# Optimization experiments

Hardware: AMD Instinct MI355X
Metric: run time of the kernel (lower is better)

## Reference

```python
import jax, jax.numpy as jnp
import numpy as np

B, T, E, H = 8, 2048, 1024, 64

def setup_inputs() -> dict:
    key = jax.random.key(0)
    ks = jax.random.split(key, 7)
    s = 1.0 / np.sqrt(E)
    return {
        "x": jax.random.normal(ks[0], (B, T, E), dtype=jnp.float32),
        "Wk": jax.random.normal(ks[1], (E, H), dtype=jnp.float32) * s,
        "bk": jax.random.normal(ks[2], (H,), dtype=jnp.float32) * 0.01,
        "Wq": jax.random.normal(ks[3], (E, H), dtype=jnp.float32) * s,
        "bq": jax.random.normal(ks[4], (H,), dtype=jnp.float32) * 0.01,
        "Wv": jax.random.normal(ks[5], (E, H), dtype=jnp.float32) * s,
        "bv": jax.random.normal(ks[6], (H,), dtype=jnp.float32) * 0.01,
    }

def reference(x, Wk, bk, Wq, bq, Wv, bv):
    # q,k,v: [B, T, H]
    k = x @ Wk + bk
    q = x @ Wq + bq
    v = x @ Wv + bv
    scale = jnp.asarray(H, x.dtype) ** -0.5
    scores = jnp.einsum('bth,bsh->bts', q, k) * scale  # [B, T, T]
    T_ = x.shape[1]
    causal = jnp.tril(jnp.ones((T_, T_), dtype=bool))
    scores = jnp.where(causal, scores, jnp.asarray(-jnp.inf, x.dtype))
    attn = jax.nn.softmax(scores, axis=-1)  # dropout p=0.0 -> identity
    return jnp.einsum('bts,bsh->bth', attn, v)
```

## Files before the change

kernel.cpp:

```cpp
#include <hip/hip_runtime.h>
#include <hip/hip_bf16.h>
#include <math.h>

#define BB 8
#define TT 2048
#define EE 1024
#define HH 64
#define QSCALE 0.18033688011112042f

typedef __attribute__((ext_vector_type(8))) short short8;
typedef __attribute__((ext_vector_type(4))) float f32x4;
typedef __attribute__((ext_vector_type(4))) unsigned short us4;

__device__ inline unsigned short f2bf(float f) {
  union { __hip_bfloat16 h; unsigned short u; } cv;
  cv.h = __float2bfloat16(f);
  return cv.u;
}

__global__ __launch_bounds__(256) void prep_w(
    const float* __restrict__ Wk, const float* __restrict__ Wq,
    const float* __restrict__ Wv, unsigned short* __restrict__ Wf) {
  const int idx = blockIdx.x * 256 + threadIdx.x;
  const int lane = idx & 63, ks = (idx >> 6) & 31, t = idx >> 11;
  const int q = lane & 15, g = lane >> 4;
  const int m = t >> 2, h = (t & 3) * 16 + q;
  const float* W = (m == 0) ? Wk : (m == 1) ? Wq : Wv;
  const float sc = (m == 1) ? QSCALE : 1.f;
  const int e0 = ks * 32 + g * 8;
  unsigned short v[8];
  #pragma unroll
  for (int j = 0; j < 8; ++j) v[j] = f2bf(W[(e0 + j) * 64 + h] * sc);
  *(short8*)&Wf[(size_t)idx * 8] = *(short8*)v;
}

__global__ __launch_bounds__(256) void qkv_proj(
    const float* __restrict__ x,
    const float* __restrict__ bk, const float* __restrict__ bq,
    const float* __restrict__ bv, const unsigned short* __restrict__ Wf,
    unsigned short* __restrict__ kf, unsigned short* __restrict__ qf,
    unsigned short* __restrict__ vf) {
  __shared__ alignas(16) unsigned short xs[2][32][264];

  const int tid = threadIdx.x;
  const long row0 = (long)blockIdx.x * 32;
  const int w = tid >> 6, lane = tid & 63;
  const int q = lane & 15, g = lane >> 4;

  const float4* xg = (const float4*)&x[row0 * EE];

  #pragma unroll
  for (int i = 0; i < 8; ++i) {
    const int flat = i * 256 + tid;
    const int rr = flat >> 6, c4 = flat & 63;
    const float4 xv = xg[rr * 256 + c4];
    us4 pk = {f2bf(xv.x), f2bf(xv.y), f2bf(xv.z), f2bf(xv.w)};
    *(us4*)&xs[0][rr][c4 * 4] = pk;
  }
  __syncthreads();

  const f32x4 z = {0.f, 0.f, 0.f, 0.f};
  f32x4 acc00 = z, acc01 = z, acc02 = z;
  f32x4 acc10 = z, acc11 = z, acc12 = z;
  const unsigned short* wf0 = &Wf[(size_t)(3 * w) * 16384 + (size_t)lane * 8];

  float4 st[8];
  #pragma unroll
  for (int cc = 0; cc < 4; ++cc) {
    if (cc < 3) {
      #pragma unroll
      for (int i = 0; i < 8; ++i) {
        const int flat = i * 256 + tid;
        const int rr = flat >> 6, c4 = flat & 63;
        st[i] = xg[rr * 256 + (cc + 1) * 64 + c4];
      }
    }
    #pragma unroll
    for (int ksl = 0; ksl < 8; ++ksl) {
      const short8 a0 = *(const short8*)&xs[cc & 1][q][ksl * 32 + g * 8];
      const short8 a1 = *(const short8*)&xs[cc & 1][16 + q][ksl * 32 + g * 8];
      const int ks = cc * 8 + ksl;
      const short8 b0 = *(const short8*)&wf0[ks * 512];
      const short8 b1 = *(const short8*)&wf0[16384 + ks * 512];
      const short8 b2 = *(const short8*)&wf0[32768 + ks * 512];
      acc00 = __builtin_amdgcn_mfma_f32_16x16x32_bf16(a0, b0, acc00, 0, 0, 0);
      acc10 = __builtin_amdgcn_mfma_f32_16x16x32_bf16(a1, b0, acc10, 0, 0, 0);
      acc01 = __builtin_amdgcn_mfma_f32_16x16x32_bf16(a0, b1, acc01, 0, 0, 0);
      acc11 = __builtin_amdgcn_mfma_f32_16x16x32_bf16(a1, b1, acc11, 0, 0, 0);
      acc02 = __builtin_amdgcn_mfma_f32_16x16x32_bf16(a0, b2, acc02, 0, 0, 0);
      acc12 = __builtin_amdgcn_mfma_f32_16x16x32_bf16(a1, b2, acc12, 0, 0, 0);
    }
    if (cc < 3) {
      #pragma unroll
      for (int i = 0; i < 8; ++i) {
        const int flat = i * 256 + tid;
        const int rr = flat >> 6, c4 = flat & 63;
        us4 pk = {f2bf(st[i].x), f2bf(st[i].y), f2bf(st[i].z), f2bf(st[i].w)};
        *(us4*)&xs[(cc + 1) & 1][rr][c4 * 4] = pk;
      }
    }
    __syncthreads();
  }

  const long bidx = row0 >> 11;
  const int tl0 = (int)(row0 & 2047);
  #pragma unroll
  for (int i = 0; i < 3; ++i) {
    const int tgl = 3 * w + i;
    const int mm = tgl >> 2, hb = tgl & 3;
    const int h = hb * 16 + q;
    const float bias = (mm == 0) ? bk[h] : (mm == 1) ? bq[h] * QSCALE : bv[h];
    #pragma unroll
    for (int stp = 0; stp < 2; ++stp) {
      const f32x4 a = (stp == 0) ? ((i == 0) ? acc00 : (i == 1) ? acc01 : acc02)
                                 : ((i == 0) ? acc10 : (i == 1) ? acc11 : acc12);
      #pragma unroll
      for (int r = 0; r < 4; ++r) {
        const int tl = tl0 + stp * 16 + 4 * g + r;
        const unsigned short ov = f2bf(a[r] + bias);
        if (mm == 2) {
          const size_t vidx = (size_t)bidx * 131072 + (size_t)(tl >> 5) * 2048 +
                              (size_t)(h >> 4) * 512 +
                              (size_t)((tl & 31) >> 3) * 128 +
                              (size_t)(h & 15) * 8 + (tl & 7);
          vf[vidx] = ov;
        } else {
          const size_t kqidx = (size_t)bidx * 131072 + (size_t)(tl >> 4) * 1024 +
                               (size_t)(h >> 5) * 512 +
                               (size_t)((h & 31) >> 3) * 128 +
                               (size_t)(tl & 15) * 8 + (h & 7);
          if (mm == 0) kf[kqidx] = ov; else qf[kqidx] = ov;
        }
      }
    }
  }
}

#define BODY(KC0, KC1, KC2, KC3, KN0, KN1, KN2, KN3, tt, PREF) do {          \
    const unsigned short* vp_ = vfb + (size_t)(tt) * 2048;                   \
    const short8 V0 = *(const short8*)&vp_[0];                               \
    const short8 V1 = *(const short8*)&vp_[512];                             \
    const short8 V2 = *(const short8*)&vp_[1024];                            \
    const short8 V3 = *(const short8*)&vp_[1536];                            \
    if (PREF) {                                                              \
      const unsigned short* kp_ = kfb + (size_t)((tt) + stride) * 2048;      \
      KN0 = *(const short8*)&kp_[0];                                         \
      KN1 = *(const short8*)&kp_[512];                                       \
      KN2 = *(const short8*)&kp_[1024];                                      \
      KN3 = *(const short8*)&kp_[1536];                                      \
    }                                                                        \
    f32x4 sa = __builtin_amdgcn_mfma_f32_16x16x32_bf16(KC0, Qf0, z, 0,0,0);  \
    sa = __builtin_amdgcn_mfma_f32_16x16x32_bf16(KC1, Qf1, sa, 0,0,0);       \
    f32x4 sb = __builtin_amdgcn_mfma_f32_16x16x32_bf16(KC2, Qf0, z, 0,0,0);  \
    sb = __builtin_amdgcn_mfma_f32_16x16x32_bf16(KC3, Qf1, sb, 0,0,0);       \
    const int k0_ = (tt) * 32;                                               \
    if (k0_ + 31 > q0) {                                                     \
      _Pragma("unroll")                                                      \
      for (int r = 0; r < 4; ++r) {                                          \
        if (k0_ + 4 * g + r > qg) sa[r] = -INFINITY;                         \
        if (k0_ + 16 + 4 * g + r > qg) sb[r] = -INFINITY;                    \
      }                                                                      \
    }                                                                        \
    float pmax = fmaxf(fmaxf(fmaxf(sa[0], sa[1]), fmaxf(sa[2], sa[3])),      \
                       fmaxf(fmaxf(sb[0], sb[1]), fmaxf(sb[2], sb[3])));     \
    if (!__all(pmax <= m + 8.0f)) {                                          \
      float tmax = pmax;                                                     \
      tmax = fmaxf(tmax, __shfl_xor(tmax, 16));                              \
      tmax = fmaxf(tmax, __shfl_xor(tmax, 32));                              \
      const float nm = fmaxf(m, tmax);                                       \
      const float rs = __builtin_amdgcn_exp2f(m - nm);                       \
      l *= rs; o0 *= rs; o1 *= rs; o2 *= rs; o3 *= rs;                       \
      m = nm;                                                                \
    }                                                                        \
    float ps = 0.f;                                                          \
    _Pragma("unroll")                                                        \
    for (int r = 0; r < 4; ++r) {                                            \
      sa[r] = __builtin_amdgcn_exp2f(sa[r] - m); ps += sa[r];                \
      sb[r] = __builtin_amdgcn_exp2f(sb[r] - m); ps += sb[r];                \
    }                                                                        \
    l += ps;                                                                 \
    unsigned pw0, pw1, pw2, pw3;                                             \
    asm("v_cvt_pk_bf16_f32 %0, %1, %2" : "=v"(pw0) : "v"(sa[0]), "v"(sa[1]));\
    asm("v_cvt_pk_bf16_f32 %0, %1, %2" : "=v"(pw1) : "v"(sa[2]), "v"(sa[3]));\
    asm("v_cvt_pk_bf16_f32 %0, %1, %2" : "=v"(pw2) : "v"(sb[0]), "v"(sb[1]));\
    asm("v_cvt_pk_bf16_f32 %0, %1, %2" : "=v"(pw3) : "v"(sb[2]), "v"(sb[3]));\
    const int srcA = q + ((g & 1) << 5);                                     \
    const int srcB = srcA + 16;                                              \
    const unsigned r0a = __shfl((int)pw0, srcA);                             \
    const unsigned r1a = __shfl((int)pw1, srcA);                             \
    const unsigned r2a = __shfl((int)pw2, srcA);                             \
    const unsigned r3a = __shfl((int)pw3, srcA);                             \
    const unsigned r0b = __shfl((int)pw0, srcB);                             \
    const unsigned r1b = __shfl((int)pw1, srcB);                             \
    const unsigned r2b = __shfl((int)pw2, srcB);                             \
    const unsigned r3b = __shfl((int)pw3, srcB);                             \
    union { unsigned u[4]; short8 s; } pf_;                                  \
    const bool hi_ = (g >= 2);                                               \
    pf_.u[0] = hi_ ? r2a : r0a;                                              \
    pf_.u[1] = hi_ ? r3a : r1a;                                              \
    pf_.u[2] = hi_ ? r2b : r0b;                                              \
    pf_.u[3] = hi_ ? r3b : r1b;                                              \
    const short8 Pf = pf_.s;                                                 \
    o0 = __builtin_amdgcn_mfma_f32_16x16x32_bf16(V0, Pf, o0, 0,0,0);         \
    o1 = __builtin_amdgcn_mfma_f32_16x16x32_bf16(V1, Pf, o1, 0,0,0);         \
    o2 = __builtin_amdgcn_mfma_f32_16x16x32_bf16(V2, Pf, o2, 0,0,0);         \
    o3 = __builtin_amdgcn_mfma_f32_16x16x32_bf16(V3, Pf, o3, 0,0,0);         \
  } while (0)

__global__ __launch_bounds__(512) void attn_fwd(
    const unsigned short* __restrict__ qf, const unsigned short* __restrict__ kf,
    const unsigned short* __restrict__ vf, float* __restrict__ out) {
  __shared__ float accS[8][64][17];
  __shared__ float mlS[8][2][16];

  const int tid = threadIdx.x;
  const int w = tid >> 6, lane = tid & 63;
  const int q = lane & 15, g = lane >> 4;

  const int b = blockIdx.x & 7;
  const int p = blockIdx.x >> 3;
  const int s1 = 127 - p;
  const int nt0 = (p + 2) >> 1, nt1 = (129 - p) >> 1;
  int k = (8 * nt0 + 32) / 65;
  if (k < 1) k = 1;
  if (k > 7) k = 7;

  const bool onS0 = (w < k);
  const int s = onS0 ? p : s1;
  const int nt = onS0 ? nt0 : nt1;
  const int stride = onS0 ? k : (8 - k);
  int t = onS0 ? w : (w - k);

  const int q0 = s * 16;
  const int qg = q0 + q;

  const unsigned short* kfb = kf + (size_t)b * 131072 + (size_t)lane * 8;
  const unsigned short* vfb = vf + (size_t)b * 131072 + (size_t)lane * 8;
  const unsigned short* qfb = qf + (size_t)b * 131072 + (size_t)s * 1024 +
                              (size_t)lane * 8;
  const short8 Qf0 = *(const short8*)&qfb[0];
  const short8 Qf1 = *(const short8*)&qfb[512];

  const f32x4 z = {0.f, 0.f, 0.f, 0.f};
  float m = -3.0e38f, l = 0.f;
  f32x4 o0 = z, o1 = z, o2 = z, o3 = z;

  {
    short8 A0, A1, A2, A3, B0, B1, B2, B3;
    const unsigned short* kp0 = kfb + (size_t)t * 2048;
    A0 = *(const short8*)&kp0[0];
    A1 = *(const short8*)&kp0[512];
    A2 = *(const short8*)&kp0[1024];
    A3 = *(const short8*)&kp0[1536];
    for (;;) {
      bool pf = (t + stride) < nt;
      BODY(A0, A1, A2, A3, B0, B1, B2, B3, t, pf);
      if (!pf) break;
      t += stride;
      pf = (t + stride) < nt;
      BODY(B0, B1, B2, B3, A0, A1, A2, A3, t, pf);
      if (!pf) break;
      t += stride;
    }
  }

  float lq = l;
  lq += __shfl_xor(lq, 16);
  lq += __shfl_xor(lq, 32);
  #pragma unroll
  for (int hb = 0; hb < 4; ++hb) {
    const f32x4 a = (hb == 0) ? o0 : (hb == 1) ? o1 : (hb == 2) ? o2 : o3;
    #pragma unroll
    for (int r = 0; r < 4; ++r) accS[w][16 * hb + 4 * g + r][q] = a[r];
  }
  if (g == 0) { mlS[w][0][q] = m; mlS[w][1][q] = lq; }
  __syncthreads();

  const int half = tid >> 8;
  const int sm = half ? s1 : p;
  const int lo = half ? k : 0, hi = half ? 8 : k;
  const int row = tid & 63, qq = (tid >> 6) & 3;
  const long obase = ((long)b * TT + sm * 16) * 64;
  #pragma unroll
  for (int kk = 0; kk < 4; ++kk) {
    const int qv = qq + 4 * kk;
    float M = -INFINITY;
    for (int i = lo; i < hi; ++i) M = fmaxf(M, mlS[i][0][qv]);
    float L = 0.f, acc = 0.f;
    for (int i = lo; i < hi; ++i) {
      const float fi = __builtin_amdgcn_exp2f(mlS[i][0][qv] - M);
      L += fi * mlS[i][1][qv];
      acc += fi * accS[i][row][qv];
    }
    out[obase + (long)qv * 64 + row] = acc / L;
  }
}

extern "C" void kernel_launch(void* const* d_in, const int* in_sizes, int n_in,
                              void* d_out, int out_size, void* d_ws, size_t ws_size,
                              hipStream_t stream) {
  const float* x  = (const float*)d_in[0];
  const float* Wk = (const float*)d_in[1];
  const float* bk = (const float*)d_in[2];
  const float* Wq = (const float*)d_in[3];
  const float* bq = (const float*)d_in[4];
  const float* Wv = (const float*)d_in[5];
  const float* bv = (const float*)d_in[6];
  float* out = (float*)d_out;

  unsigned short* qfb = (unsigned short*)d_ws;
  unsigned short* kfb = qfb + (size_t)1048576;
  unsigned short* vfb = kfb + (size_t)1048576;
  unsigned short* Wf  = vfb + (size_t)1048576;

  prep_w<<<dim3(96), 256, 0, stream>>>(Wk, Wq, Wv, Wf);
  qkv_proj<<<dim3(512), 256, 0, stream>>>(x, bk, bq, bv, Wf, kfb, qfb, vfb);
  attn_fwd<<<dim3(512), 512, 0, stream>>>(qfb, kfb, vfb, out);
}
```

Measured before the change: 50.36 us.

## Switch attention to 32x32x16 MFMA with 32-row query tiles

Rewrites the attention inner loop to use 32x32x16 bf16 MFMA instructions on 32-query tiles instead of 16x16x32 on 16-query tiles. The K/Q/V workspace layouts produced by the projection kernel are changed to match the new operand fragments. P is reshuffled with cross-half xor shuffles in place of general shuffles, and the block count is halved with the split-K merge adjusted. This aims for fewer instructions and shuffles per key tile and more K/V reuse per load. The costs are higher register pressure and fewer blocks, which may hurt load balance across CUs.

```diff
diff --git a/kernel.cpp b/kernel.cpp
--- a/kernel.cpp
+++ b/kernel.cpp
@@ -10,6 +10,7 @@
 
 typedef __attribute__((ext_vector_type(8))) short short8;
 typedef __attribute__((ext_vector_type(4))) float f32x4;
+typedef __attribute__((ext_vector_type(16))) float f32x16;
 typedef __attribute__((ext_vector_type(4))) unsigned short us4;
 
 __device__ inline unsigned short f2bf(float f) {
@@ -119,16 +120,17 @@
         const int tl = tl0 + stp * 16 + 4 * g + r;
         const unsigned short ov = f2bf(a[r] + bias);
         if (mm == 2) {
+          const int lane32v = ((hb & 1) * 16 + q) + 32 * ((tl >> 3) & 1);
           const size_t vidx = (size_t)bidx * 131072 + (size_t)(tl >> 5) * 2048 +
-                              (size_t)(h >> 4) * 512 +
-                              (size_t)((tl & 31) >> 3) * 128 +
-                              (size_t)(h & 15) * 8 + (tl & 7);
+                              (size_t)(hb >> 1) * 1024 +
+                              (size_t)((tl >> 4) & 1) * 512 +
+                              (size_t)lane32v * 8 + (size_t)(tl & 7);
           vf[vidx] = ov;
         } else {
-          const size_t kqidx = (size_t)bidx * 131072 + (size_t)(tl >> 4) * 1024 +
-                               (size_t)(h >> 5) * 512 +
-                               (size_t)((h & 31) >> 3) * 128 +
-                               (size_t)(tl & 15) * 8 + (h & 7);
+          const int lane32 = (tl & 31) + 32 * ((q >> 3) & 1);
+          const size_t kqidx = (size_t)bidx * 131072 + (size_t)(tl >> 5) * 2048 +
+                               (size_t)hb * 512 + (size_t)lane32 * 8 +
+                               (size_t)(q & 7);
           if (mm == 0) kf[kqidx] = ov; else qf[kqidx] = ov;
         }
       }
@@ -136,91 +138,99 @@
   }
 }
 
-#define BODY(KC0, KC1, KC2, KC3, KN0, KN1, KN2, KN3, tt, PREF) do {          \
+#define BODY(KC, KN, tt, PREF) do {                                          \
     const unsigned short* vp_ = vfb + (size_t)(tt) * 2048;                   \
-    const short8 V0 = *(const short8*)&vp_[0];                               \
-    const short8 V1 = *(const short8*)&vp_[512];                             \
-    const short8 V2 = *(const short8*)&vp_[1024];                            \
-    const short8 V3 = *(const short8*)&vp_[1536];                            \
+    const short8 V00 = *(const short8*)&vp_[0];                              \
+    const short8 V01 = *(const short8*)&vp_[512];                            \
+    const short8 V10 = *(const short8*)&vp_[1024];                           \
+    const short8 V11 = *(const short8*)&vp_[1536];                           \
     if (PREF) {                                                              \
       const unsigned short* kp_ = kfb + (size_t)((tt) + stride) * 2048;      \
-      KN0 = *(const short8*)&kp_[0];                                         \
-      KN1 = *(const short8*)&kp_[512];                                       \
-      KN2 = *(const short8*)&kp_[1024];                                      \
-      KN3 = *(const short8*)&kp_[1536];                                      \
-    }                                                                        \
-    f32x4 sa = __builtin_amdgcn_mfma_f32_16x16x32_bf16(KC0, Qf0, z, 0,0,0);  \
-    sa = __builtin_amdgcn_mfma_f32_16x16x32_bf16(KC1, Qf1, sa, 0,0,0);       \
-    f32x4 sb = __builtin_amdgcn_mfma_f32_16x16x32_bf16(KC2, Qf0, z, 0,0,0);  \
-    sb = __builtin_amdgcn_mfma_f32_16x16x32_bf16(KC3, Qf1, sb, 0,0,0);       \
+      KN[0] = *(const short8*)&kp_[0];                                       \
+      KN[1] = *(const short8*)&kp_[512];                                     \
+      KN[2] = *(const short8*)&kp_[1024];                                    \
+      KN[3] = *(const short8*)&kp_[1536];                                    \
+    }                                                                        \
+    f32x16 S;                                                                \
+    _Pragma("unroll")                                                        \
+    for (int r = 0; r < 16; ++r) S[r] = 0.f;                                 \
+    S = __builtin_amdgcn_mfma_f32_32x32x16_bf16(KC[0], Qf0, S, 0, 0, 0);     \
+    S = __builtin_amdgcn_mfma_f32_32x32x16_bf16(KC[1], Qf1, S, 0, 0, 0);     \
+    S = __builtin_amdgcn_mfma_f32_32x32x16_bf16(KC[2], Qf2, S, 0, 0, 0);     \
+    S = __builtin_amdgcn_mfma_f32_32x32x16_bf16(KC[3], Qf3, S, 0, 0, 0);     \
     const int k0_ = (tt) * 32;                                               \
     if (k0_ + 31 > q0) {                                                     \
       _Pragma("unroll")                                                      \
-      for (int r = 0; r < 4; ++r) {                                          \
-        if (k0_ + 4 * g + r > qg) sa[r] = -INFINITY;                         \
-        if (k0_ + 16 + 4 * g + r > qg) sb[r] = -INFINITY;                    \
+      for (int r = 0; r < 16; ++r) {                                         \
+        const int key = (r & 3) + 8 * (r >> 2) + 4 * hf;                     \
+        if (k0_ + key > qg) S[r] = -INFINITY;                                \
       }                                                                      \
     }                                                                        \
-    float pmax = fmaxf(fmaxf(fmaxf(sa[0], sa[1]), fmaxf(sa[2], sa[3])),      \
-                       fmaxf(fmaxf(sb[0], sb[1]), fmaxf(sb[2], sb[3])));     \
+    float pmax = S[0];                                                       \
+    _Pragma("unroll")                                                        \
+    for (int r = 1; r < 16; ++r) pmax = fmaxf(pmax, S[r]);                   \
     if (!__all(pmax <= m + 8.0f)) {                                          \
-      float tmax = pmax;                                                     \
-      tmax = fmaxf(tmax, __shfl_xor(tmax, 16));                              \
-      tmax = fmaxf(tmax, __shfl_xor(tmax, 32));                              \
-      const float nm = fmaxf(m, tmax);                                       \
+      const float pm2 = fmaxf(pmax, __shfl_xor(pmax, 32));                   \
+      const float nm = fmaxf(m, pm2);                                        \
       const float rs = __builtin_amdgcn_exp2f(m - nm);                       \
-      l *= rs; o0 *= rs; o1 *= rs; o2 *= rs; o3 *= rs;                       \
+      l *= rs;                                                               \
+      _Pragma("unroll")                                                      \
+      for (int r = 0; r < 16; ++r) { O0[r] *= rs; O1[r] *= rs; }             \
       m = nm;                                                                \
     }                                                                        \
-    float ps = 0.f;                                                          \
+    float P[16]; float ps = 0.f;                                             \
     _Pragma("unroll")                                                        \
-    for (int r = 0; r < 4; ++r) {                                            \
-      sa[r] = __builtin_amdgcn_exp2f(sa[r] - m); ps += sa[r];                \
-      sb[r] = __builtin_amdgcn_exp2f(sb[r] - m); ps += sb[r];                \
+    for (int r = 0; r < 16; ++r) {                                           \
+      P[r] = __builtin_amdgcn_exp2f(S[r] - m); ps += P[r];                   \
     }                                                                        \
     l += ps;                                                                 \
-    unsigned pw0, pw1, pw2, pw3;                                             \
-    asm("v_cvt_pk_bf16_f32 %0, %1, %2" : "=v"(pw0) : "v"(sa[0]), "v"(sa[1]));\
-    asm("v_cvt_pk_bf16_f32 %0, %1, %2" : "=v"(pw1) : "v"(sa[2]), "v"(sa[3]));\
-    asm("v_cvt_pk_bf16_f32 %0, %1, %2" : "=v"(pw2) : "v"(sb[0]), "v"(sb[1]));\
-    asm("v_cvt_pk_bf16_f32 %0, %1, %2" : "=v"(pw3) : "v"(sb[2]), "v"(sb[3]));\
-    const int srcA = q + ((g & 1) << 5);                                     \
-    const int srcB = srcA + 16;                                              \
-    const unsigned r0a = __shfl((int)pw0, srcA);                             \
-    const unsigned r1a = __shfl((int)pw1, srcA);                             \
-    const unsigned r2a = __shfl((int)pw2, srcA);                             \
-    const unsigned r3a = __shfl((int)pw3, srcA);                             \
-    const unsigned r0b = __shfl((int)pw0, srcB);                             \
-    const unsigned r1b = __shfl((int)pw1, srcB);                             \
-    const unsigned r2b = __shfl((int)pw2, srcB);                             \
-    const unsigned r3b = __shfl((int)pw3, srcB);                             \
-    union { unsigned u[4]; short8 s; } pf_;                                  \
-    const bool hi_ = (g >= 2);                                               \
-    pf_.u[0] = hi_ ? r2a : r0a;                                              \
-    pf_.u[1] = hi_ ? r3a : r1a;                                              \
-    pf_.u[2] = hi_ ? r2b : r0b;                                              \
-    pf_.u[3] = hi_ ? r3b : r1b;                                              \
-    const short8 Pf = pf_.s;                                                 \
-    o0 = __builtin_amdgcn_mfma_f32_16x16x32_bf16(V0, Pf, o0, 0,0,0);         \
-    o1 = __builtin_amdgcn_mfma_f32_16x16x32_bf16(V1, Pf, o1, 0,0,0);         \
-    o2 = __builtin_amdgcn_mfma_f32_16x16x32_bf16(V2, Pf, o2, 0,0,0);         \
-    o3 = __builtin_amdgcn_mfma_f32_16x16x32_bf16(V3, Pf, o3, 0,0,0);         \
+    unsigned wa0, wa1, wa2, wa3, wb0, wb1, wb2, wb3;                         \
+    asm("v_cvt_pk_bf16_f32 %0, %1, %2" : "=v"(wa0) : "v"(P[0]), "v"(P[1])); \
+    asm("v_cvt_pk_bf16_f32 %0, %1, %2" : "=v"(wb0) : "v"(P[2]), "v"(P[3])); \
+    asm("v_cvt_pk_bf16_f32 %0, %1, %2" : "=v"(wa1) : "v"(P[4]), "v"(P[5])); \
+    asm("v_cvt_pk_bf16_f32 %0, %1, %2" : "=v"(wb1) : "v"(P[6]), "v"(P[7])); \
+    asm("v_cvt_pk_bf16_f32 %0, %1, %2" : "=v"(wa2) : "v"(P[8]), "v"(P[9])); \
+    asm("v_cvt_pk_bf16_f32 %0, %1, %2" : "=v"(wb2) : "v"(P[10]), "v"(P[11]));\
+    asm("v_cvt_pk_bf16_f32 %0, %1, %2" : "=v"(wa3) : "v"(P[12]), "v"(P[13]));\
+    asm("v_cvt_pk_bf16_f32 %0, %1, %2" : "=v"(wb3) : "v"(P[14]), "v"(P[15]));\
+    {            \
+      const unsigned sA = hf ? wa1 : wa0, sB = hf ? wb1 : wb0;               \
+      const unsigned tA = hf ? wa0 : wa1, tB = hf ? wb0 : wb1;               \
+      const unsigned xA = __shfl_xor((int)tA, 32);                           \
+      const unsigned xB = __shfl_xor((int)tB, 32);                           \
+      union { unsigned u[4]; short8 s; } pf_;                                \
+      pf_.u[0] = hf ? xA : sA; pf_.u[1] = hf ? xB : sB;                      \
+      pf_.u[2] = hf ? sA : xA; pf_.u[3] = hf ? sB : xB;                      \
+      O0 = __builtin_amdgcn_mfma_f32_32x32x16_bf16(V00, pf_.s, O0, 0, 0, 0); \
+      O1 = __builtin_amdgcn_mfma_f32_32x32x16_bf16(V10, pf_.s, O1, 0, 0, 0); \
+    }                                                                        \
+    {                                                  \
+      const unsigned sA = hf ? wa3 : wa2, sB = hf ? wb3 : wb2;               \
+      const unsigned tA = hf ? wa2 : wa3, tB = hf ? wb2 : wb3;               \
+      const unsigned xA = __shfl_xor((int)tA, 32);                           \
+      const unsigned xB = __shfl_xor((int)tB, 32);                           \
+      union { unsigned u[4]; short8 s; } pf_;                                \
+      pf_.u[0] = hf ? xA : sA; pf_.u[1] = hf ? xB : sB;                      \
+      pf_.u[2] = hf ? sA : xA; pf_.u[3] = hf ? sB : xB;                      \
+      O0 = __builtin_amdgcn_mfma_f32_32x32x16_bf16(V01, pf_.s, O0, 0, 0, 0); \
+      O1 = __builtin_amdgcn_mfma_f32_32x32x16_bf16(V11, pf_.s, O1, 0, 0, 0); \
+    }                                                                        \
   } while (0)
 
 __global__ __launch_bounds__(512) void attn_fwd(
     const unsigned short* __restrict__ qf, const unsigned short* __restrict__ kf,
     const unsigned short* __restrict__ vf, float* __restrict__ out) {
-  __shared__ float accS[8][64][17];
-  __shared__ float mlS[8][2][16];
+  __shared__ float accS[8][32][65];
+  __shared__ float mlS[8][2][32];
 
   const int tid = threadIdx.x;
   const int w = tid >> 6, lane = tid & 63;
-  const int q = lane & 15, g = lane >> 4;
+  const int q = lane & 31, hf = lane >> 5;
 
   const int b = blockIdx.x & 7;
   const int p = blockIdx.x >> 3;
-  const int s1 = 127 - p;
-  const int nt0 = (p + 2) >> 1, nt1 = (129 - p) >> 1;
+  const int s1 = 63 - p;
+  const int nt0 = p + 1, nt1 = 64 - p;
   int k = (8 * nt0 + 32) / 65;
   if (k < 1) k = 1;
   if (k > 7) k = 7;
@@ -231,68 +241,70 @@
   const int stride = onS0 ? k : (8 - k);
   int t = onS0 ? w : (w - k);
 
-  const int q0 = s * 16;
+  const int q0 = s * 32;
   const int qg = q0 + q;
 
   const unsigned short* kfb = kf + (size_t)b * 131072 + (size_t)lane * 8;
   const unsigned short* vfb = vf + (size_t)b * 131072 + (size_t)lane * 8;
-  const unsigned short* qfb = qf + (size_t)b * 131072 + (size_t)s * 1024 +
+  const unsigned short* qfb = qf + (size_t)b * 131072 + (size_t)s * 2048 +
                               (size_t)lane * 8;
   const short8 Qf0 = *(const short8*)&qfb[0];
   const short8 Qf1 = *(const short8*)&qfb[512];
-
-  const f32x4 z = {0.f, 0.f, 0.f, 0.f};
+  const short8 Qf2 = *(const short8*)&qfb[1024];
+  const short8 Qf3 = *(const short8*)&qfb[1536];
+
   float m = -3.0e38f, l = 0.f;
-  f32x4 o0 = z, o1 = z, o2 = z, o3 = z;
+  f32x16 O0, O1;
+  #pragma unroll
+  for (int r = 0; r < 16; ++r) { O0[r] = 0.f; O1[r] = 0.f; }
 
   {
-    short8 A0, A1, A2, A3, B0, B1, B2, B3;
+    short8 A[4], B[4];
     const unsigned short* kp0 = kfb + (size_t)t * 2048;
-    A0 = *(const short8*)&kp0[0];
-    A1 = *(const short8*)&kp0[512];
-    A2 = *(const short8*)&kp0[1024];
-    A3 = *(const short8*)&kp0[1536];
+    A[0] = *(const short8*)&kp0[0];
+    A[1] = *(const short8*)&kp0[512];
+    A[2] = *(const short8*)&kp0[1024];
+    A[3] = *(const short8*)&kp0[1536];
     for (;;) {
       bool pf = (t + stride) < nt;
-      BODY(A0, A1, A2, A3, B0, B1, B2, B3, t, pf);
+      BODY(A, B, t, pf);
       if (!pf) break;
       t += stride;
       pf = (t + stride) < nt;
-      BODY(B0, B1, B2, B3, A0, A1, A2, A3, t, pf);
+      BODY(B, A, t, pf);
       if (!pf) break;
       t += stride;
     }
   }
 
-  float lq = l;
-  lq += __shfl_xor(lq, 16);
-  lq += __shfl_xor(lq, 32);
-  #pragma unroll
-  for (int hb = 0; hb < 4; ++hb) {
-    const f32x4 a = (hb == 0) ? o0 : (hb == 1) ? o1 : (hb == 2) ? o2 : o3;
-    #pragma unroll
-    for (int r = 0; r < 4; ++r) accS[w][16 * hb + 4 * g + r][q] = a[r];
-  }
-  if (g == 0) { mlS[w][0][q] = m; mlS[w][1][q] = lq; }
+  const float lq = l + __shfl_xor(l, 32);
+  #pragma unroll
+  for (int r = 0; r < 16; ++r) {
+    const int hh0 = (r & 3) + 8 * (r >> 2) + 4 * hf;
+    accS[w][q][hh0] = O0[r];
+    accS[w][q][hh0 + 32] = O1[r];
+  }
+  if (hf == 0) { mlS[w][0][q] = m; mlS[w][1][q] = lq; }
   __syncthreads();
 
-  const int half = tid >> 8;
-  const int sm = half ? s1 : p;
-  const int lo = half ? k : 0, hi = half ? 8 : k;
-  const int row = tid & 63, qq = (tid >> 6) & 3;
-  const long obase = ((long)b * TT + sm * 16) * 64;
-  #pragma unroll
-  for (int kk = 0; kk < 4; ++kk) {
-    const int qv = qq + 4 * kk;
+  const int half_t = tid >> 8;
+  const int sm = half_t ? s1 : p;
+  const int lo = half_t ? k : 0, hi2 = half_t ? 8 : k;
+  const int hh = tid & 63;
+  const int qb0 = (tid >> 6) & 3;
+  const long obase = ((long)b * TT + (long)sm * 32) * 64;
+  #pragma unroll
+  for (int kk = 0; kk < 8; ++kk) {
+    const int qv = qb0 + 4 * kk;
     float M = -INFINITY;
-    for (int i = lo; i < hi; ++i) M = fmaxf(M, mlS[i][0][qv]);
+    for (int i = lo; i < hi2; ++i) M = fmaxf(M, mlS[i][0][qv]);
     float L = 0.f, acc = 0.f;
-    for (int i = lo; i < hi; ++i) {
+    for (int i = lo; i < hi2; ++i) {
       const float fi = __builtin_amdgcn_exp2f(mlS[i][0][qv] - M);
       L += fi * mlS[i][1][qv];
-      acc += fi * accS[i][row][qv];
-    }
-    out[obase + (long)qv * 64 + row] = acc / L;
+      acc += fi * accS[i][qv][hh];
+    }
+    out[obase + (long)qv * 64 + hh] = acc / L;
   }
 }
 
@@ -315,5 +327,5 @@
 
   prep_w<<<dim3(96), 256, 0, stream>>>(Wk, Wq, Wv, Wf);
   qkv_proj<<<dim3(512), 256, 0, stream>>>(x, bk, bq, bv, Wf, kfb, qfb, vfb);
-  attn_fwd<<<dim3(512), 512, 0, stream>>>(qfb, kfb, vfb, out);
-}
+  attn_fwd<<<dim3(256), 512, 0, stream>>>(qfb, kfb, vfb, out);
+}
```

Result: no change. 51.32 us (+1.9%).

## Stage QKV outputs in LDS for coalesced stores and shrink x staging chunks

Applied to the files above, without the earlier changes.

The projection kernel now writes its bf16 K/Q/V fragments into a shared-memory image and then emits them with coalesced 16-byte stores, replacing scattered 2-byte global stores. The x staging buffer is halved to 128-column chunks over 8 non-unrolled iterations with fewer prefetch registers, which lowers LDS and register use and may raise occupancy. It adds an extra barrier and LDS round trip, and the rolled loop may schedule loads less aggressively.

```diff
diff --git a/kernel.cpp b/kernel.cpp
--- a/kernel.cpp
+++ b/kernel.cpp
@@ -40,7 +40,8 @@
     const float* __restrict__ bv, const unsigned short* __restrict__ Wf,
     unsigned short* __restrict__ kf, unsigned short* __restrict__ qf,
     unsigned short* __restrict__ vf) {
-  __shared__ alignas(16) unsigned short xs[2][32][264];
+  __shared__ alignas(16) unsigned short xs2[2][32][136];
+  __shared__ alignas(16) unsigned short img[6144];
 
   const int tid = threadIdx.x;
   const long row0 = (long)blockIdx.x * 32;
@@ -48,14 +49,14 @@
   const int q = lane & 15, g = lane >> 4;
 
   const float4* xg = (const float4*)&x[row0 * EE];
-
-  #pragma unroll
-  for (int i = 0; i < 8; ++i) {
-    const int flat = i * 256 + tid;
-    const int rr = flat >> 6, c4 = flat & 63;
+  const int rrl = tid >> 5, c4 = tid & 31;
+
+  #pragma unroll
+  for (int i = 0; i < 4; ++i) {
+    const int rr = i * 8 + rrl;
     const float4 xv = xg[rr * 256 + c4];
     us4 pk = {f2bf(xv.x), f2bf(xv.y), f2bf(xv.z), f2bf(xv.w)};
-    *(us4*)&xs[0][rr][c4 * 4] = pk;
+    *(us4*)&xs2[0][rr][c4 * 4] = pk;
   }
   __syncthreads();
 
@@ -64,22 +65,21 @@
   f32x4 acc10 = z, acc11 = z, acc12 = z;
   const unsigned short* wf0 = &Wf[(size_t)(3 * w) * 16384 + (size_t)lane * 8];
 
-  float4 st[8];
-  #pragma unroll
-  for (int cc = 0; cc < 4; ++cc) {
-    if (cc < 3) {
-      #pragma unroll
-      for (int i = 0; i < 8; ++i) {
-        const int flat = i * 256 + tid;
-        const int rr = flat >> 6, c4 = flat & 63;
-        st[i] = xg[rr * 256 + (cc + 1) * 64 + c4];
-      }
+  #pragma unroll 1
+  for (int cc = 0; cc < 8; ++cc) {
+    float4 st0, st1, st2, st3;
+    if (cc < 7) {
+      const int cb = (cc + 1) * 32 + c4;
+      st0 = xg[(0 * 8 + rrl) * 256 + cb];
+      st1 = xg[(1 * 8 + rrl) * 256 + cb];
+      st2 = xg[(2 * 8 + rrl) * 256 + cb];
+      st3 = xg[(3 * 8 + rrl) * 256 + cb];
     }
     #pragma unroll
-    for (int ksl = 0; ksl < 8; ++ksl) {
-      const short8 a0 = *(const short8*)&xs[cc & 1][q][ksl * 32 + g * 8];
-      const short8 a1 = *(const short8*)&xs[cc & 1][16 + q][ksl * 32 + g * 8];
-      const int ks = cc * 8 + ksl;
+    for (int ksl = 0; ksl < 4; ++ksl) {
+      const int ks = cc * 4 + ksl;
+      const short8 a0 = *(const short8*)&xs2[cc & 1][q][ksl * 32 + g * 8];
+      const short8 a1 = *(const short8*)&xs2[cc & 1][16 + q][ksl * 32 + g * 8];
       const short8 b0 = *(const short8*)&wf0[ks * 512];
       const short8 b1 = *(const short8*)&wf0[16384 + ks * 512];
       const short8 b2 = *(const short8*)&wf0[32768 + ks * 512];
@@ -90,20 +90,20 @@
       acc02 = __builtin_amdgcn_mfma_f32_16x16x32_bf16(a0, b2, acc02, 0, 0, 0);
       acc12 = __builtin_amdgcn_mfma_f32_16x16x32_bf16(a1, b2, acc12, 0, 0, 0);
     }
-    if (cc < 3) {
-      #pragma unroll
-      for (int i = 0; i < 8; ++i) {
-        const int flat = i * 256 + tid;
-        const int rr = flat >> 6, c4 = flat & 63;
-        us4 pk = {f2bf(st[i].x), f2bf(st[i].y), f2bf(st[i].z), f2bf(st[i].w)};
-        *(us4*)&xs[(cc + 1) & 1][rr][c4 * 4] = pk;
-      }
-    }
-    __syncthreads();
-  }
-
-  const long bidx = row0 >> 11;
-  const int tl0 = (int)(row0 & 2047);
+    if (cc < 7) {
+      const int nb = (cc + 1) & 1;
+      us4 p0 = {f2bf(st0.x), f2bf(st0.y), f2bf(st0.z), f2bf(st0.w)};
+      us4 p1 = {f2bf(st1.x), f2bf(st1.y), f2bf(st1.z), f2bf(st1.w)};
+      us4 p2 = {f2bf(st2.x), f2bf(st2.y), f2bf(st2.z), f2bf(st2.w)};
+      us4 p3 = {f2bf(st3.x), f2bf(st3.y), f2bf(st3.z), f2bf(st3.w)};
+      *(us4*)&xs2[nb][0 * 8 + rrl][c4 * 4] = p0;
+      *(us4*)&xs2[nb][1 * 8 + rrl][c4 * 4] = p1;
+      *(us4*)&xs2[nb][2 * 8 + rrl][c4 * 4] = p2;
+      *(us4*)&xs2[nb][3 * 8 + rrl][c4 * 4] = p3;
+      __syncthreads();
+    }
+  }
+
   #pragma unroll
   for (int i = 0; i < 3; ++i) {
     const int tgl = 3 * w + i;
@@ -116,24 +116,28 @@
                                  : ((i == 0) ? acc10 : (i == 1) ? acc11 : acc12);
       #pragma unroll
       for (int r = 0; r < 4; ++r) {
-        const int tl = tl0 + stp * 16 + 4 * g + r;
+        const int tlh = 4 * g + r;
         const unsigned short ov = f2bf(a[r] + bias);
         if (mm == 2) {
-          const size_t vidx = (size_t)bidx * 131072 + (size_t)(tl >> 5) * 2048 +
-                              (size_t)(h >> 4) * 512 +
-                              (size_t)((tl & 31) >> 3) * 128 +
-                              (size_t)(h & 15) * 8 + (tl & 7);
-          vf[vidx] = ov;
+          img[4096 + hb * 512 + (stp * 2 + (tlh >> 3)) * 128 + q * 8 +
+              (tlh & 7)] = ov;
         } else {
-          const size_t kqidx = (size_t)bidx * 131072 + (size_t)(tl >> 4) * 1024 +
-                               (size_t)(h >> 5) * 512 +
-                               (size_t)((h & 31) >> 3) * 128 +
-                               (size_t)(tl & 15) * 8 + (h & 7);
-          if (mm == 0) kf[kqidx] = ov; else qf[kqidx] = ov;
+          const int g2 = (h & 31) >> 3;
+          img[mm * 2048 + stp * 1024 + (h >> 5) * 512 + g2 * 128 + tlh * 8 +
+              (h & 7)] = ov;
         }
       }
     }
   }
+  __syncthreads();
+
+  const long bidx = row0 >> 11;
+  const int tlg = (int)(row0 & 2047);
+  const size_t b16 = (size_t)bidx * 131072 + (size_t)(tlg >> 4) * 1024;
+  const size_t b32 = (size_t)bidx * 131072 + (size_t)(tlg >> 5) * 2048;
+  *(short8*)&kf[b16 + (size_t)tid * 8] = *(const short8*)&img[tid * 8];
+  *(short8*)&qf[b16 + (size_t)tid * 8] = *(const short8*)&img[2048 + tid * 8];
+  *(short8*)&vf[b32 + (size_t)tid * 8] = *(const short8*)&img[4096 + tid * 8];
 }
 
 #define BODY(KC0, KC1, KC2, KC3, KN0, KN1, KN2, KN3, tt, PREF) do {          \
```

Result: faster. 48.71 us (-3.3%).
